# Kernel tuning notes

Measured on AMD Instinct MI355X. Metric: run time of the kernel, lower is better.

## Reference

```python
import math
import jax, jax.numpy as jnp
import numpy as np

B, CIN, COUT, K, S = 2, 64, 64, 3, 18  # batch, channels, kernel size per dim, spatial size per dim


def setup_inputs() -> dict:
    key = jax.random.key(0)
    k1, k2 = jax.random.split(key)
    inputs = jax.random.normal(k1, (B, CIN, S, S, S, S), dtype=jnp.float32)
    std = 1.0 / math.sqrt(CIN * K ** 4)  # matches init_weight: 1/sqrt(in_channels * n_offsets)
    kernel = jax.random.uniform(k2, (K ** 4, CIN, COUT), dtype=jnp.float32, minval=-std, maxval=std)
    return {"inputs": inputs, "kernel": kernel}


def reference(inputs, kernel):
    # kernel: [k0*k1*k2*k3, Cin, Cout], offsets enumerated row-major over the 4 kernel dims.
    # Equivalent to the per-offset matmul + shift-accumulate in conv4d (valid padding,
    # stride=1, dilation=1), expressed as a single 4-spatial-dim XLA convolution.
    cin, cout = kernel.shape[1], kernel.shape[2]
    w = kernel.reshape(K, K, K, K, cin, cout).transpose(5, 4, 0, 1, 2, 3)  # OIWXYZ
    out = jax.lax.conv_general_dilated(
        inputs, w,
        window_strides=(1, 1, 1, 1),
        padding='VALID',
        rhs_dilation=(1, 1, 1, 1),
        dimension_numbers=('NCWXYZ', 'OIWXYZ', 'NCWXYZ'),
    )  # [B, Cout, 16, 16, 16, 16]
    return out
```

## Files before the change

### kernel.cpp

```cpp
#include <hip/hip_runtime.h>


typedef __attribute__((ext_vector_type(8))) short bf16x8;
typedef __attribute__((ext_vector_type(4))) float f32x4;
typedef __attribute__((ext_vector_type(8))) unsigned short ushort8;
typedef unsigned short u16;
typedef unsigned int u32;

#define S_OFF_BYTES 663552u
#define WS_NEEDED   27537408u

__device__ __forceinline__ u16 f2bf(float f) {
    u32 u = __float_as_uint(f);
    u += 0x7FFFu + ((u >> 16) & 1u);
    return (u16)(u >> 16);
}

__global__ __launch_bounds__(256) void wprep(const float* __restrict__ ker, u16* __restrict__ wg) {
    const int g = blockIdx.x * 256 + threadIdx.x;
    const int l = g & 63, ks = (g >> 6) & 1, rt = (g >> 7) & 3, off = g >> 9;
    const int co  = rt * 16 + (l & 15);
    const int ci0 = ks * 32 + (l >> 4) * 8;
    const float* p = ker + (size_t)off * 4096 + co;
    ushort8 v;
#pragma unroll
    for (int e = 0; e < 8; ++e) v[e] = f2bf(p[(size_t)(ci0 + e) * 64]);
    *(ushort8*)(wg + (size_t)g * 8) = v;
}

__global__ __launch_bounds__(256) void sprep(const float* __restrict__ in, u16* __restrict__ s) {
    __shared__ u16 L[64 * 330];
    const int blk = blockIdx.x;
    const int b = blk / 324, wx = blk - b * 324;
    const float* src = in + (size_t)b * 6718464 + (wx / 18) * 5832 + (wx % 18) * 324;
    const int t = threadIdx.x;
    for (int i = t; i < 5184; i += 256) {
        const int ci = i / 81, j = i - ci * 81;
        float4 v = *(const float4*)(src + (size_t)ci * 104976 + j * 4);
        u32* q = (u32*)&L[ci * 330 + j * 4];
        q[0] = f2bf(v.x) | ((u32)f2bf(v.y) << 16);
        q[1] = f2bf(v.z) | ((u32)f2bf(v.w) << 16);
    }
    __syncthreads();
    u16* dst = s + (size_t)blk * 20736;
    for (int i = t; i < 2592; i += 256) {
        const int ks = i / 1296, r4 = i - ks * 1296;
        const int rem = r4 >> 2, g = r4 & 3;
        ushort8 v;
#pragma unroll
        for (int e = 0; e < 8; ++e) v[e] = L[(ks * 32 + g * 8 + e) * 330 + rem];
        const int gp = g ^ ((rem >> 1) & 3);
        *(ushort8*)(dst + ks * 10368 + rem * 32 + gp * 8) = v;
    }
}

__global__ __launch_bounds__(128, 1)
void conv4d_main(const u16* __restrict__ wg, const u16* __restrict__ s, float* __restrict__ out) {
    __shared__ u16 Bs[2][10368];

    const int bid = blockIdx.x;
    const int bs  = (bid & 7) * 64 + (bid >> 3);
    const int b   = bs >> 8;
    const int w   = (bs >> 4) & 15;
    const int x   = bs & 15;

    const int t  = threadIdx.x, wv = t >> 6, l = t & 63;
    const int lg = l >> 4, ll = l & 15;

    f32x4 acc[4][8];
#pragma unroll
    for (int i = 0; i < 4; ++i)
#pragma unroll
        for (int j = 0; j < 8; ++j) acc[i][j] = (f32x4){0.f, 0.f, 0.f, 0.f};

    const u16* sb = s + (size_t)(b * 324 + w * 18 + x) * 20736;

    bf16x8 af[2][3][4];
    bf16x8 bb[2][10];

#define STAGE_B(h)                                                                       \
    do {                                                                                 \
        const int kwx_ = (h) >> 1, ks_ = (h) & 1;                                        \
        const int kw_ = kwx_ / 3, kx_ = kwx_ - kw_ * 3;                                  \
        const u16* src_ = sb + (size_t)(kw_ * 18 + kx_) * 20736 + ks_ * 10368;           \
        const int base_ = wv * 648;                                                      \
        _Pragma("unroll")                                                                \
        for (int k_ = 0; k_ < 10; ++k_) {                                                \
            const int i_ = base_ + k_ * 64 + l;                                          \
            __builtin_amdgcn_global_load_lds(                                            \
                (const __attribute__((address_space(1))) u32*)(src_ + (size_t)i_ * 8),   \
                (__attribute__((address_space(3))) u32*)&Bs[(h) & 1][i_ * 8], 16, 0, 0); \
        }                                                                                \
        if (l < 8) {                                                                     \
            const int i_ = base_ + 640 + l;                                              \
            __builtin_amdgcn_global_load_lds(                                            \
                (const __attribute__((address_space(1))) u32*)(src_ + (size_t)i_ * 8),   \
                (__attribute__((address_space(3))) u32*)&Bs[(h) & 1][i_ * 8], 16, 0, 0); \
        }                                                                                \
    } while (0)

#define LOAD_AF(BK, U)                                                                   \
    do {                                                                                 \
        const int tk_ = (U) / 3, kz_ = (U) % 3;                                          \
        const int kwx_ = tk_ >> 1, ks_ = tk_ & 1;                                        \
        _Pragma("unroll")                                                                \
        for (int ky_ = 0; ky_ < 3; ++ky_)                                                \
            _Pragma("unroll")                                                            \
            for (int rt_ = 0; rt_ < 4; ++rt_)                                            \
                af[BK][ky_][rt_] = *(const bf16x8*)(wg                                   \
                    + (size_t)(kwx_ * 9 + ky_ * 3 + kz_) * 4096                          \
                    + (size_t)(rt_ * 2 + ks_) * 512 + l * 8);                            \
    } while (0)

#define READ_BB(BK, P, KZ)                                                               \
    do {                                                                                 \
        const u16* Tb_ = Bs[(P) & 1];                                                    \
        _Pragma("unroll")                                                                \
        for (int j_ = 0; j_ < 10; ++j_) {                                                \
            const int rem_ = (8 * wv + j_) * 18 + ll + (KZ);                             \
            bb[BK][j_] = *(const bf16x8*)&Tb_[rem_ * 32 + ((lg ^ ((rem_ >> 1) & 3)) << 3)]; \
        }                                                                                \
    } while (0)

#define MFMA96(BK)                                                                       \
    do {                                                                                 \
        __builtin_amdgcn_s_setprio(1);                                                   \
        _Pragma("unroll")                                                                \
        for (int ky_ = 0; ky_ < 3; ++ky_)                                                \
            _Pragma("unroll")                                                            \
            for (int ct_ = 0; ct_ < 8; ++ct_)                                            \
                _Pragma("unroll")                                                        \
                for (int rt_ = 0; rt_ < 4; ++rt_)                                        \
                    acc[rt_][ct_] = __builtin_amdgcn_mfma_f32_16x16x32_bf16(             \
                        af[BK][ky_][rt_], bb[BK][ct_ + ky_], acc[rt_][ct_], 0, 0, 0);    \
        __builtin_amdgcn_s_setprio(0);                                                   \
    } while (0)

    STAGE_B(0);
    LOAD_AF(0, 0);
    asm volatile("s_waitcnt vmcnt(0)" ::: "memory");
    __builtin_amdgcn_sched_barrier(0);
    __builtin_amdgcn_s_barrier();

    for (int u6 = 0; u6 < 54; u6 += 6) {
#pragma unroll
        for (int m = 0; m < 6; ++m) {
            const int u = u6 + m;
            const int p = u / 3;
            const int q = m % 3;
            const int cur = m & 1, nxt = cur ^ 1;
            if (q == 0) READ_BB(cur, p, 0);
            if (q == 0 && p + 1 < 18) STAGE_B(p + 1);
            if (u + 1 < 54) LOAD_AF(nxt, u + 1);
            if (q < 2) READ_BB(nxt, p, q + 1);
            MFMA96(cur);
            if (q == 2 && u < 53) {
                asm volatile("s_waitcnt vmcnt(0)" ::: "memory");
                __builtin_amdgcn_sched_barrier(0);
                __builtin_amdgcn_s_barrier();
            }
        }
    }
#undef STAGE_B
#undef LOAD_AF
#undef READ_BB
#undef MFMA96

    float* ob = out + (size_t)b * 4194304 + (size_t)w * 4096 + (size_t)x * 256;
#pragma unroll
    for (int rt = 0; rt < 4; ++rt) {
        const int co0 = rt * 16 + 4 * lg;
#pragma unroll
        for (int ct = 0; ct < 8; ++ct) {
            const int base = (8 * wv + ct) * 16 + ll;
#pragma unroll
            for (int r = 0; r < 4; ++r)
                ob[(size_t)(co0 + r) * 65536 + base] = acc[rt][ct][r];
        }
    }
}

__global__ __launch_bounds__(512, 2)
void conv4d_mfma(const float* __restrict__ in, const float* __restrict__ ker,
                 float* __restrict__ out) {
    __shared__ unsigned short T[18 * 18 * 64];
    __shared__ unsigned short Wt[2][64 * 64];
    const int bx = blockIdx.x;
    const int b = bx >> 8, wsp = (bx >> 4) & 15, x = bx & 15;
    const int t = threadIdx.x, wv = t >> 6, l = t & 63;
    const int lg = l >> 4, ll = l & 15;
    const float* inb = in + (size_t)b * 6718464 + wsp * 5832 + x * 324;
    f32x4 acc[4][2];
#pragma unroll
    for (int i = 0; i < 4; ++i)
#pragma unroll
        for (int j = 0; j < 2; ++j) acc[i][j] = (f32x4){0.f, 0.f, 0.f, 0.f};
#pragma unroll
    for (int f0 = 0; f0 < 4096; f0 += 512) {
        const int f = f0 + t, ci = f >> 6, co = f & 63;
        Wt[0][co * 64 + ((((ci >> 3) ^ (co & 7)) << 3) | (ci & 7))] = f2bf(ker[f]);
    }
    for (int off = 0; off < 81; ++off) {
        const int sub = off % 9;
        if (sub == 0) {
            const int kw = off / 27, kx = (off / 9) % 3;
            const float* p = inb + kw * 5832 + kx * 324;
            for (int f = t; f < 18 * 18 * 64; f += 512) {
                const int ci = f / 324, rem = f - ci * 324, zp = rem % 18;
                T[rem * 64 + ((((ci >> 3) ^ (zp & 7)) << 3) | (ci & 7))] =
                    f2bf(p[(size_t)ci * 104976 + rem]);
            }
        }
        if (off + 1 < 81) {
            const float* p = ker + (off + 1) * 4096;
            unsigned short* wb = Wt[(off + 1) & 1];
#pragma unroll
            for (int f0 = 0; f0 < 4096; f0 += 512) {
                const int f = f0 + t, ci = f >> 6, co = f & 63;
                wb[co * 64 + ((((ci >> 3) ^ (co & 7)) << 3) | (ci & 7))] = f2bf(p[f]);
            }
        }
        if (sub == 0) __syncthreads();
        const int ky = sub / 3, kz = sub - ky * 3;
        const int zp = ll + kz, zs = zp & 7;
#pragma unroll
        for (int ks = 0; ks < 2; ++ks) {
            bf16x8 af[4];
#pragma unroll
            for (int rt = 0; rt < 4; ++rt)
                af[rt] = *(const bf16x8*)&Wt[off & 1][(rt * 16 + ll) * 64 + (((lg + 4 * ks) ^ (ll & 7)) << 3)];
#pragma unroll
            for (int ct = 0; ct < 2; ++ct) {
                const int rem = (2 * wv + ct + ky) * 18 + zp;
                const bf16x8 bfr = *(const bf16x8*)&T[rem * 64 + (((lg + 4 * ks) ^ zs) << 3)];
#pragma unroll
                for (int rt = 0; rt < 4; ++rt)
                    acc[rt][ct] = __builtin_amdgcn_mfma_f32_16x16x32_bf16(af[rt], bfr, acc[rt][ct], 0, 0, 0);
            }
        }
        __syncthreads();
    }
    float* ob = out + (size_t)b * 4194304 + wsp * 4096 + x * 256;
#pragma unroll
    for (int rt = 0; rt < 4; ++rt) {
        const int co0 = rt * 16 + 4 * lg;
#pragma unroll
        for (int ct = 0; ct < 2; ++ct) {
            const int base = (2 * wv + ct) * 16 + ll;
#pragma unroll
            for (int r = 0; r < 4; ++r)
                ob[(size_t)(co0 + r) * 65536 + base] = acc[rt][ct][r];
        }
    }
}

extern "C" void kernel_launch(void* const* d_in, const int* in_sizes, int n_in,
                              void* d_out, int out_size, void* d_ws, size_t ws_size,
                              hipStream_t stream) {
    const float* in  = (const float*)d_in[0];
    const float* ker = (const float*)d_in[1];
    float* out = (float*)d_out;
    if (ws_size >= (size_t)WS_NEEDED) {
        u16* wg = (u16*)d_ws;
        u16* s  = (u16*)((char*)d_ws + S_OFF_BYTES);
        wprep<<<dim3(162), dim3(256), 0, stream>>>(ker, wg);
        sprep<<<dim3(648), dim3(256), 0, stream>>>(in, s);
        conv4d_main<<<dim3(512), dim3(128), 0, stream>>>(wg, s, out);
    } else {
        conv4d_mfma<<<dim3(512), dim3(512), 0, stream>>>(in, ker, out);
    }
}
```

Baseline: 92.40 us.

## Split main conv block into four waves over channel halves and merge prep kernels

Merges the weight and input preparation kernels into one launch so a kernel launch boundary goes away. The main conv kernel now uses 256 threads (four waves) instead of 128, with each wave computing half the output channels for half the spatial rows. Per-wave accumulator and A-fragment register counts are halved, and staging of each B tile is spread across four waves. B fragments are no longer double-buffered, and the barrier wait is relaxed to vmcnt(6), so in-flight A loads can overlap the barrier. In exchange, each block reads the same B data from LDS twice, and ordering is looser.

```diff
diff --git a/kernel.cpp b/kernel.cpp
--- a/kernel.cpp
+++ b/kernel.cpp
@@ -16,24 +16,26 @@
     return (u16)(u >> 16);
 }
 
-__global__ __launch_bounds__(256) void wprep(const float* __restrict__ ker, u16* __restrict__ wg) {
-    const int g = blockIdx.x * 256 + threadIdx.x;
-    const int l = g & 63, ks = (g >> 6) & 1, rt = (g >> 7) & 3, off = g >> 9;
-    const int co  = rt * 16 + (l & 15);
-    const int ci0 = ks * 32 + (l >> 4) * 8;
-    const float* p = ker + (size_t)off * 4096 + co;
-    ushort8 v;
-#pragma unroll
-    for (int e = 0; e < 8; ++e) v[e] = f2bf(p[(size_t)(ci0 + e) * 64]);
-    *(ushort8*)(wg + (size_t)g * 8) = v;
-}
-
-__global__ __launch_bounds__(256) void sprep(const float* __restrict__ in, u16* __restrict__ s) {
+__global__ __launch_bounds__(256) void prep(const float* __restrict__ in,
+                                            const float* __restrict__ ker,
+                                            u16* __restrict__ s, u16* __restrict__ wg) {
+    const int blk = blockIdx.x;
+    const int t = threadIdx.x;
+    if (blk >= 648) {
+        const int g = (blk - 648) * 256 + t;
+        const int l = g & 63, ks = (g >> 6) & 1, rt = (g >> 7) & 3, off = g >> 9;
+        const int co  = rt * 16 + (l & 15);
+        const int ci0 = ks * 32 + (l >> 4) * 8;
+        const float* p = ker + (size_t)off * 4096 + co;
+        ushort8 v;
+#pragma unroll
+        for (int e = 0; e < 8; ++e) v[e] = f2bf(p[(size_t)(ci0 + e) * 64]);
+        *(ushort8*)(wg + (size_t)g * 8) = v;
+        return;
+    }
     __shared__ u16 L[64 * 330];
-    const int blk = blockIdx.x;
     const int b = blk / 324, wx = blk - b * 324;
     const float* src = in + (size_t)b * 6718464 + (wx / 18) * 5832 + (wx % 18) * 324;
-    const int t = threadIdx.x;
     for (int i = t; i < 5184; i += 256) {
         const int ci = i / 81, j = i - ci * 81;
         float4 v = *(const float4*)(src + (size_t)ci * 104976 + j * 4);
@@ -54,9 +56,9 @@
     }
 }
 
-__global__ __launch_bounds__(128, 1)
+__global__ __launch_bounds__(256, 1)
 void conv4d_main(const u16* __restrict__ wg, const u16* __restrict__ s, float* __restrict__ out) {
-    __shared__ u16 Bs[2][10368];
+    __shared__ u16 Bq[2][10368];
 
     const int bid = blockIdx.x;
     const int bs  = (bid & 7) * 64 + (bid >> 3);
@@ -66,63 +68,65 @@
 
     const int t  = threadIdx.x, wv = t >> 6, l = t & 63;
     const int lg = l >> 4, ll = l & 15;
-
-    f32x4 acc[4][8];
-#pragma unroll
-    for (int i = 0; i < 4; ++i)
+    const int ch = wv >> 1;
+    const int sh = wv & 1;
+
+    f32x4 acc[2][8];
+#pragma unroll
+    for (int i = 0; i < 2; ++i)
 #pragma unroll
         for (int j = 0; j < 8; ++j) acc[i][j] = (f32x4){0.f, 0.f, 0.f, 0.f};
 
     const u16* sb = s + (size_t)(b * 324 + w * 18 + x) * 20736;
 
-    bf16x8 af[2][3][4];
-    bf16x8 bb[2][10];
+    bf16x8 af[2][6];
+    bf16x8 bb[10];
+
+#define LOAD_A(BK, U)                                                                    \
+    do {                                                                                 \
+        const int tk_ = (U) / 3, kz_ = (U) % 3;                                          \
+        const int kwx_ = tk_ >> 1, ks_ = tk_ & 1;                                        \
+        _Pragma("unroll")                                                                \
+        for (int ky_ = 0; ky_ < 3; ++ky_)                                                \
+            _Pragma("unroll")                                                            \
+            for (int rt_ = 0; rt_ < 2; ++rt_)                                            \
+                af[BK][ky_ * 2 + rt_] = *(const bf16x8*)(wg                              \
+                    + (size_t)(kwx_ * 9 + ky_ * 3 + kz_) * 4096                          \
+                    + (size_t)(2 * ch + rt_) * 1024 + ks_ * 512 + l * 8);                \
+    } while (0)
 
 #define STAGE_B(h)                                                                       \
     do {                                                                                 \
         const int kwx_ = (h) >> 1, ks_ = (h) & 1;                                        \
         const int kw_ = kwx_ / 3, kx_ = kwx_ - kw_ * 3;                                  \
         const u16* src_ = sb + (size_t)(kw_ * 18 + kx_) * 20736 + ks_ * 10368;           \
-        const int base_ = wv * 648;                                                      \
-        _Pragma("unroll")                                                                \
-        for (int k_ = 0; k_ < 10; ++k_) {                                                \
+        const int base_ = wv * 324;                                                      \
+        _Pragma("unroll")                                                                \
+        for (int k_ = 0; k_ < 5; ++k_) {                                                 \
             const int i_ = base_ + k_ * 64 + l;                                          \
             __builtin_amdgcn_global_load_lds(                                            \
                 (const __attribute__((address_space(1))) u32*)(src_ + (size_t)i_ * 8),   \
-                (__attribute__((address_space(3))) u32*)&Bs[(h) & 1][i_ * 8], 16, 0, 0); \
+                (__attribute__((address_space(3))) u32*)&Bq[(h) & 1][i_ * 8], 16, 0, 0); \
         }                                                                                \
-        if (l < 8) {                                                                     \
-            const int i_ = base_ + 640 + l;                                              \
+        if (l < 4) {                                                                     \
+            const int i_ = base_ + 320 + l;                                              \
             __builtin_amdgcn_global_load_lds(                                            \
                 (const __attribute__((address_space(1))) u32*)(src_ + (size_t)i_ * 8),   \
-                (__attribute__((address_space(3))) u32*)&Bs[(h) & 1][i_ * 8], 16, 0, 0); \
+                (__attribute__((address_space(3))) u32*)&Bq[(h) & 1][i_ * 8], 16, 0, 0); \
         }                                                                                \
     } while (0)
 
-#define LOAD_AF(BK, U)                                                                   \
-    do {                                                                                 \
-        const int tk_ = (U) / 3, kz_ = (U) % 3;                                          \
-        const int kwx_ = tk_ >> 1, ks_ = tk_ & 1;                                        \
-        _Pragma("unroll")                                                                \
-        for (int ky_ = 0; ky_ < 3; ++ky_)                                                \
-            _Pragma("unroll")                                                            \
-            for (int rt_ = 0; rt_ < 4; ++rt_)                                            \
-                af[BK][ky_][rt_] = *(const bf16x8*)(wg                                   \
-                    + (size_t)(kwx_ * 9 + ky_ * 3 + kz_) * 4096                          \
-                    + (size_t)(rt_ * 2 + ks_) * 512 + l * 8);                            \
-    } while (0)
-
-#define READ_BB(BK, P, KZ)                                                               \
-    do {                                                                                 \
-        const u16* Tb_ = Bs[(P) & 1];                                                    \
+#define READ_B(TKPAR, KZ)                                                                \
+    do {                                                                                 \
+        const u16* Tb_ = Bq[TKPAR];                                                      \
         _Pragma("unroll")                                                                \
         for (int j_ = 0; j_ < 10; ++j_) {                                                \
-            const int rem_ = (8 * wv + j_) * 18 + ll + (KZ);                             \
-            bb[BK][j_] = *(const bf16x8*)&Tb_[rem_ * 32 + ((lg ^ ((rem_ >> 1) & 3)) << 3)]; \
+            const int rem_ = (8 * sh + j_) * 18 + ll + (KZ);                             \
+            bb[j_] = *(const bf16x8*)&Tb_[rem_ * 32 + ((lg ^ ((rem_ >> 1) & 3)) << 3)];  \
         }                                                                                \
     } while (0)
 
-#define MFMA96(BK)                                                                       \
+#define MFMA48(ABK)                                                                      \
     do {                                                                                 \
         __builtin_amdgcn_s_setprio(1);                                                   \
         _Pragma("unroll")                                                                \
@@ -130,14 +134,14 @@
             _Pragma("unroll")                                                            \
             for (int ct_ = 0; ct_ < 8; ++ct_)                                            \
                 _Pragma("unroll")                                                        \
-                for (int rt_ = 0; rt_ < 4; ++rt_)                                        \
+                for (int rt_ = 0; rt_ < 2; ++rt_)                                        \
                     acc[rt_][ct_] = __builtin_amdgcn_mfma_f32_16x16x32_bf16(             \
-                        af[BK][ky_][rt_], bb[BK][ct_ + ky_], acc[rt_][ct_], 0, 0, 0);    \
+                        af[ABK][ky_ * 2 + rt_], bb[ct_ + ky_], acc[rt_][ct_], 0, 0, 0);  \
         __builtin_amdgcn_s_setprio(0);                                                   \
     } while (0)
 
+    LOAD_A(0, 0);
     STAGE_B(0);
-    LOAD_AF(0, 0);
     asm volatile("s_waitcnt vmcnt(0)" ::: "memory");
     __builtin_amdgcn_sched_barrier(0);
     __builtin_amdgcn_s_barrier();
@@ -149,30 +153,30 @@
             const int p = u / 3;
             const int q = m % 3;
             const int cur = m & 1, nxt = cur ^ 1;
-            if (q == 0) READ_BB(cur, p, 0);
+            if (u + 1 < 54) LOAD_A(nxt, u + 1);
             if (q == 0 && p + 1 < 18) STAGE_B(p + 1);
-            if (u + 1 < 54) LOAD_AF(nxt, u + 1);
-            if (q < 2) READ_BB(nxt, p, q + 1);
-            MFMA96(cur);
+            READ_B(p & 1, q);
+            __builtin_amdgcn_sched_barrier(0);
+            MFMA48(cur);
             if (q == 2 && u < 53) {
-                asm volatile("s_waitcnt vmcnt(0)" ::: "memory");
+                asm volatile("s_waitcnt vmcnt(6)" ::: "memory");
                 __builtin_amdgcn_sched_barrier(0);
                 __builtin_amdgcn_s_barrier();
             }
         }
     }
+#undef LOAD_A
 #undef STAGE_B
-#undef LOAD_AF
-#undef READ_BB
-#undef MFMA96
+#undef READ_B
+#undef MFMA48
 
     float* ob = out + (size_t)b * 4194304 + (size_t)w * 4096 + (size_t)x * 256;
 #pragma unroll
-    for (int rt = 0; rt < 4; ++rt) {
-        const int co0 = rt * 16 + 4 * lg;
+    for (int rt = 0; rt < 2; ++rt) {
+        const int co0 = ch * 32 + rt * 16 + 4 * lg;
 #pragma unroll
         for (int ct = 0; ct < 8; ++ct) {
-            const int base = (8 * wv + ct) * 16 + ll;
+            const int base = (8 * sh + ct) * 16 + ll;
 #pragma unroll
             for (int r = 0; r < 4; ++r)
                 ob[(size_t)(co0 + r) * 65536 + base] = acc[rt][ct][r];
@@ -263,9 +267,8 @@
     if (ws_size >= (size_t)WS_NEEDED) {
         u16* wg = (u16*)d_ws;
         u16* s  = (u16*)((char*)d_ws + S_OFF_BYTES);
-        wprep<<<dim3(162), dim3(256), 0, stream>>>(ker, wg);
-        sprep<<<dim3(648), dim3(256), 0, stream>>>(in, s);
-        conv4d_main<<<dim3(512), dim3(128), 0, stream>>>(wg, s, out);
+        prep<<<dim3(810), dim3(256), 0, stream>>>(in, ker, s, wg);
+        conv4d_main<<<dim3(512), dim3(256), 0, stream>>>(wg, s, out);
     } else {
         conv4d_mfma<<<dim3(512), dim3(512), 0, stream>>>(in, ker, out);
     }
```

Result: faster. 86.64 us, median of 3 (-6.2%).
